# Performance work log

Measured on AMD Instinct MI355X. Metric: run time of the kernel, lower is better.

The kernel has to match this reference:

```python
import jax, jax.numpy as jnp
import numpy as np

LAMBDA = 25.0
MU = 25.0
NU = 1.0
ALPHA = 0.25
EPS = 1e-4
NUM_MATCHES = (20, 4)


def _cdist(x, y):
    # x: (B, L1, C), y: (B, L2, C) -> (B, L1, L2) euclidean distances
    x2 = jnp.sum(x * x, axis=-1)[..., :, None]
    y2 = jnp.sum(y * y, axis=-1)[..., None, :]
    d2 = x2 + y2 - 2.0 * jnp.einsum('blc,bmc->blm', x, y)
    return jnp.sqrt(jnp.maximum(d2, 0.0))


def _nearest_neighbors(input_maps, candidate_maps, distances, num_matches):
    # For each input location, its nearest candidate; then keep the
    # num_matches input locations with smallest NN distance, in original order.
    nn_dist = jnp.min(distances, axis=-1)    # (B, L1)
    nn_idx = jnp.argmin(distances, axis=-1)  # (B, L1)
    _, sel = jax.lax.top_k(-nn_dist, num_matches)  # (B, M) smallest distances
    sel = jnp.sort(sel, axis=1)  # restore original ordering of positions
    filtered_input = jnp.take_along_axis(input_maps, sel[..., None], axis=1)
    nn_sel = jnp.take_along_axis(nn_idx, sel, axis=1)
    filtered_candidate = jnp.take_along_axis(candidate_maps, nn_sel[..., None], axis=1)
    return filtered_input, filtered_candidate


def _mse(a, b):
    return jnp.mean((a - b) ** 2)


def _vicreg_loss(z_a, z_b):
    inv_loss = _mse(z_a, z_b)

    def var_loss(z):
        std = jnp.sqrt(jnp.var(z, axis=0, ddof=1) + EPS)
        return jnp.mean(jax.nn.relu(1.0 - std))

    def cov_loss(z):
        n, d = z.shape
        zc = z - jnp.mean(z, axis=0)
        cov = (zc.T @ zc) / (n - 1)
        off = cov - jnp.diag(jnp.diag(cov))
        return jnp.sum(off ** 2) / d

    v = 0.5 * (var_loss(z_a) + var_loss(z_b))
    c = cov_loss(z_a) + cov_loss(z_b)
    return LAMBDA * inv_loss + MU * v + NU * c


def _local_loss(z_global, z_local, grid_global, grid_local):
    B = z_global.shape[0]
    zg = z_global.reshape(B, -1, z_global.shape[-1])   # (B, Lg, C)
    zl = z_local.reshape(B, -1, z_local.shape[-1])     # (B, Ll, C)

    inv_loss = 0.0
    # feature-space NN
    gf, gn = _nearest_neighbors(zg, zl, _cdist(zg, zl), NUM_MATCHES[0])
    lf, ln = _nearest_neighbors(zl, zg, _cdist(zl, zg), NUM_MATCHES[1])
    inv_loss = inv_loss + (_mse(gf, gn) / 2 + _mse(lf, ln) / 2)

    # grid-space NN (distances from grids, gather from feature maps)
    gg = grid_global.reshape(B, -1, 2)
    gl = grid_local.reshape(B, -1, 2)
    gf, gn = _nearest_neighbors(zg, zl, _cdist(gg, gl), NUM_MATCHES[0])
    lf, ln = _nearest_neighbors(zl, zg, _cdist(gl, gg), NUM_MATCHES[1])
    inv_loss = inv_loss + (_mse(gf, gn) / 2 + _mse(lf, ln) / 2)

    return LAMBDA * inv_loss


def setup_inputs() -> dict:
    key = jax.random.key(0)
    ks = jax.random.split(key, 6)
    B, D, C = 32, 8192, 512
    return {
        'z_global': jax.random.normal(ks[0], (B, D), jnp.float32),
        'z_local': jax.random.normal(ks[1], (B, D), jnp.float32),
        'z_global_local_features': jax.random.normal(ks[2], (B, 24, 24, C), jnp.float32),
        'z_local_local_features': jax.random.normal(ks[3], (B, 16, 16, C), jnp.float32),
        'grid_global': jax.random.uniform(ks[4], (B, 24, 24, 2), jnp.float32),
        'grid_local': jax.random.uniform(ks[5], (B, 16, 16, 2), jnp.float32),
    }


def reference(z_global, z_local, z_global_local_features, z_local_local_features, grid_global, grid_local):
    global_loss = _vicreg_loss(z_global, z_local)
    local_loss = _local_loss(z_global_local_features, z_local_local_features, grid_global, grid_local)
    return ALPHA * global_loss + (1.0 - ALPHA) * local_loss
```

## Files before the change

### kernel.cpp

```cpp
#include <hip/hip_runtime.h>
#include <hip/hip_bf16.h>

#define BATCH 32
#define DZ    8192
#define LG    576
#define LL    256
#define CH    512

#define OFF_S      0
#define OFF_BSUM   8192
#define OFF_SELSUM 9472
#define OFF_DONE   10496
#define OFF_RNP    10560
#define OFF_CNP    305472
#define WS_NEED    895296

typedef __attribute__((ext_vector_type(8))) short bf16x8;
typedef __attribute__((ext_vector_type(4))) float f32x4;

__device__ __forceinline__ unsigned short f2bf(float x) {
  union { __hip_bfloat16 h; unsigned short u; } cv;
  cv.h = __float2bfloat16(x);
  return cv.u;
}

__device__ __forceinline__ uint4 pack8(float4 lo, float4 hi) {
  union { unsigned short h[8]; uint4 u; } pk;
  pk.h[0] = f2bf(lo.x); pk.h[1] = f2bf(lo.y); pk.h[2] = f2bf(lo.z); pk.h[3] = f2bf(lo.w);
  pk.h[4] = f2bf(hi.x); pk.h[5] = f2bf(hi.y); pk.h[6] = f2bf(hi.z); pk.h[7] = f2bf(hi.w);
  return pk.u;
}

__device__ __forceinline__ float dot4(float4 v) {
  return v.x * v.x + v.y * v.y + v.z * v.z + v.w * v.w;
}

struct SelSmem {
  unsigned long long keys[LG];
  unsigned int nnm[LG];
  float cxy[2 * LG];
  unsigned int plist[40];
  unsigned int cnt;
  float fred[4];
};

template <int V>
__device__ __forceinline__ void sel_case(
    SelSmem& sm, int b,
    const float* __restrict__ zgf, const float* __restrict__ zlf,
    const float* __restrict__ gg, const float* __restrict__ gl,
    const unsigned long long* __restrict__ rowNNp,
    const unsigned long long* __restrict__ colNNp,
    double* __restrict__ selsum) {
  constexpr bool GDIR = (V == 0 || V == 2);
  constexpr int L1 = GDIR ? LG : LL;
  constexpr int L2 = GDIR ? LL : LG;
  constexpr int M  = GDIR ? 20 : 4;
  constexpr int NR = (L1 + 255) / 256;
  const float* fin  = GDIR ? zgf + (size_t)b * LG * CH : zlf + (size_t)b * LL * CH;
  const float* fcan = GDIR ? zlf + (size_t)b * LL * CH : zgf + (size_t)b * LG * CH;
  int tid = threadIdx.x, lane = tid & 63, wv = tid >> 6;
  if (tid == 0) sm.cnt = 0;

  if constexpr (V < 2) {
    constexpr int P = (V == 0) ? 2 : 9;
    const unsigned long long* src =
        (V == 0) ? rowNNp + (size_t)b * LG * 2 : colNNp + (size_t)b * LL * 9;
    #pragma unroll
    for (int s = 0; s < NR; ++s) {
      int l = tid + s * 256;
      if (l < L1) {
        const unsigned long long* q = src + (size_t)l * P;
        unsigned long long p = q[0];
        #pragma unroll
        for (int u = 1; u < P; ++u) { unsigned long long t2 = q[u]; p = t2 < p ? t2 : p; }
        sm.keys[l] = (p & 0xFFFFFFFF00000000ull) | (unsigned)l;
        sm.nnm[l] = (unsigned)(p & 0xFFFFFFFFu);
      }
    }
  } else {
    const float* gin  = (V == 2) ? gg + (size_t)b * LG * 2 : gl + (size_t)b * LL * 2;
    const float* gcan = (V == 2) ? gl + (size_t)b * LL * 2 : gg + (size_t)b * LG * 2;
    #pragma unroll
    for (int s = 0; s < (2 * L2 + 255) / 256; ++s) {
      int i = tid + s * 256;
      if (i < 2 * L2) sm.cxy[i] = gcan[i];
    }
    __syncthreads();
    float x[NR], y[NR], bd[NR];
    unsigned bi[NR];
    #pragma unroll
    for (int s = 0; s < NR; ++s) {
      int l = tid + s * 256;
      x[s] = (l < L1) ? gin[2 * l] : 0.f;
      y[s] = (l < L1) ? gin[2 * l + 1] : 0.f;
      bd[s] = 3.4e38f; bi[s] = 0;
    }
    const float2* c2 = (const float2*)sm.cxy;
    for (int m2 = 0; m2 < L2; m2 += 8) {
      float2 cc[8];
      #pragma unroll
      for (int u = 0; u < 8; ++u) cc[u] = c2[m2 + u];
      #pragma unroll
      for (int u = 0; u < 8; ++u)
        #pragma unroll
        for (int s = 0; s < NR; ++s) {
          float dx = x[s] - cc[u].x, dy = y[s] - cc[u].y;
          float d2 = dx * dx + dy * dy;
          if (d2 < bd[s]) { bd[s] = d2; bi[s] = (unsigned)(m2 + u); }
        }
    }
    #pragma unroll
    for (int s = 0; s < NR; ++s) {
      int l = tid + s * 256;
      if (l < L1) {
        sm.keys[l] = ((unsigned long long)__float_as_uint(bd[s]) << 32) | (unsigned)l;
        sm.nnm[l] = bi[s];
      }
    }
  }
  __syncthreads();

  unsigned long long myk[NR];
  int rk[NR];
  #pragma unroll
  for (int s = 0; s < NR; ++s) {
    int l = tid + s * 256;
    myk[s] = (l < L1) ? sm.keys[l] : ~0ull;
    rk[s] = 0;
  }
  for (int j = 0; j < L1; j += 8) {
    unsigned long long kk[8];
    #pragma unroll
    for (int u = 0; u < 8; ++u) kk[u] = sm.keys[j + u];
    #pragma unroll
    for (int u = 0; u < 8; ++u)
      #pragma unroll
      for (int s = 0; s < NR; ++s) rk[s] += (kk[u] < myk[s]) ? 1 : 0;
  }
  #pragma unroll
  for (int s = 0; s < NR; ++s) {
    int l = tid + s * 256;
    if (l < L1 && rk[s] < M) {
      unsigned slot = atomicAdd(&sm.cnt, 1u);
      sm.plist[2 * slot] = (unsigned)l;
      sm.plist[2 * slot + 1] = sm.nnm[l];
    }
  }
  __syncthreads();

  float part = 0.f;
  #pragma unroll
  for (int rr = 0; rr < M / 4; ++rr) {
    int r = wv + rr * 4;
    const float4* a4 = (const float4*)(fin + (size_t)sm.plist[2 * r] * CH);
    const float4* c4 = (const float4*)(fcan + (size_t)sm.plist[2 * r + 1] * CH);
    float4 xa = a4[lane * 2], xb = a4[lane * 2 + 1];
    float4 ya = c4[lane * 2], yb = c4[lane * 2 + 1];
    float d0 = xa.x - ya.x, d1 = xa.y - ya.y, d2 = xa.z - ya.z, d3 = xa.w - ya.w;
    float d4 = xb.x - yb.x, d5 = xb.y - yb.y, d6 = xb.z - yb.z, d7 = xb.w - yb.w;
    part += d0 * d0 + d1 * d1 + d2 * d2 + d3 * d3 +
            d4 * d4 + d5 * d5 + d6 * d6 + d7 * d7;
  }
  for (int s = 32; s; s >>= 1) part += __shfl_down(part, s);
  if (lane == 0) sm.fred[wv] = part;
  __syncthreads();
  if (tid == 0)
    selsum[V * 32 + b] = (double)(sm.fred[0] + sm.fred[1] + sm.fred[2] + sm.fred[3]);
}

__global__ __launch_bounds__(256) void k_mega(
    const float* __restrict__ za, const float* __restrict__ zb,
    const float* __restrict__ zgf, const float* __restrict__ zlf,
    const float* __restrict__ gg, const float* __restrict__ gl,
    double* __restrict__ bsum, float* __restrict__ S,
    unsigned long long* __restrict__ rowNNp, unsigned long long* __restrict__ colNNp,
    double* __restrict__ selsum, unsigned int* __restrict__ doneCnt) {
  __shared__ __align__(16) char smem[28416];
  int tid = threadIdx.x, lane = tid & 63, wv = tid >> 6;
  int blk = blockIdx.x;

  if (blk < 576) {
    int fs = (blk & 7) * 72 + (blk >> 3);
    int b = fs / 18, rr_ = fs % 18;
    int by = rr_ / 9, bx = rr_ % 9;
    int row0 = bx * 64, col0 = by * 128;

    unsigned short (*As)[72] = (unsigned short(*)[72])smem;
    unsigned short (*Bs)[72] = (unsigned short(*)[72])(smem + 9216);
    float* Asn = (float*)(smem + 27648);
    float* Bsn = (float*)(smem + 27904);

    const int m16 = lane & 15, quad = lane >> 4;
    const int wm = wv >> 1, wn = wv & 1;
    const float* Ag = zgf + ((size_t)(b * LG + row0)) * CH;
    const float* Bg = zlf + ((size_t)(b * LL + col0)) * CH;
    const int sr = tid >> 2, sq = tid & 3;
    const int br = tid >> 1, bq = tid & 1;

    f32x4 acc[2][4] = {};
    float ssA = 0.f, ssB = 0.f;

    for (int k0 = 0; k0 < CH; k0 += 64) {
      const float* ap = Ag + (size_t)sr * CH + k0 + sq * 16;
      float4 a0 = *(const float4*)(ap);
      float4 a1 = *(const float4*)(ap + 4);
      float4 a2 = *(const float4*)(ap + 8);
      float4 a3 = *(const float4*)(ap + 12);
      const float* bp = Bg + (size_t)br * CH + k0 + bq * 16;
      float4 b0 = *(const float4*)(bp);
      float4 b1 = *(const float4*)(bp + 4);
      float4 b2 = *(const float4*)(bp + 8);
      float4 b3 = *(const float4*)(bp + 12);
      float4 b4 = *(const float4*)(bp + 32);
      float4 b5 = *(const float4*)(bp + 36);
      float4 b6 = *(const float4*)(bp + 40);
      float4 b7 = *(const float4*)(bp + 44);
      ssA += dot4(a0) + dot4(a1) + dot4(a2) + dot4(a3);
      ssB += dot4(b0) + dot4(b1) + dot4(b2) + dot4(b3) +
             dot4(b4) + dot4(b5) + dot4(b6) + dot4(b7);
      __syncthreads();
      *(uint4*)&As[sr][sq * 16]      = pack8(a0, a1);
      *(uint4*)&As[sr][sq * 16 + 8]  = pack8(a2, a3);
      *(uint4*)&Bs[br][bq * 16]      = pack8(b0, b1);
      *(uint4*)&Bs[br][bq * 16 + 8]  = pack8(b2, b3);
      *(uint4*)&Bs[br][bq * 16 + 32] = pack8(b4, b5);
      *(uint4*)&Bs[br][bq * 16 + 40] = pack8(b6, b7);
      __syncthreads();
      #pragma unroll
      for (int kk = 0; kk < 64; kk += 32) {
        bf16x8 af0 = *(const bf16x8*)&As[wm * 32 + m16][kk + quad * 8];
        bf16x8 af1 = *(const bf16x8*)&As[wm * 32 + 16 + m16][kk + quad * 8];
        bf16x8 bfv[4];
        #pragma unroll
        for (int j = 0; j < 4; ++j)
          bfv[j] = *(const bf16x8*)&Bs[wn * 64 + j * 16 + m16][kk + quad * 8];
        #pragma unroll
        for (int j = 0; j < 4; ++j) {
          acc[0][j] = __builtin_amdgcn_mfma_f32_16x16x32_bf16(af0, bfv[j], acc[0][j], 0, 0, 0);
          acc[1][j] = __builtin_amdgcn_mfma_f32_16x16x32_bf16(af1, bfv[j], acc[1][j], 0, 0, 0);
        }
      }
    }

    ssA += __shfl_xor(ssA, 1); ssA += __shfl_xor(ssA, 2);
    ssB += __shfl_xor(ssB, 1);
    if (sq == 0) Asn[sr] = ssA;
    if (bq == 0) Bsn[br] = ssB;
    __syncthreads();

    float na[2][4], nb[4];
    #pragma unroll
    for (int i = 0; i < 2; ++i)
      #pragma unroll
      for (int r = 0; r < 4; ++r)
        na[i][r] = Asn[wm * 32 + i * 16 + quad * 4 + r];
    #pragma unroll
    for (int j = 0; j < 4; ++j)
      nb[j] = Bsn[wn * 64 + j * 16 + m16];

    #pragma unroll
    for (int i = 0; i < 2; ++i) {
      #pragma unroll
      for (int r = 0; r < 4; ++r) {
        unsigned long long p = ~0ull;
        #pragma unroll
        for (int j = 0; j < 4; ++j) {
          float d = fmaxf(na[i][r] + nb[j] - 2.f * acc[i][j][r], 0.f);
          unsigned c = (unsigned)(col0 + wn * 64 + j * 16 + m16);
          unsigned long long pj = (((unsigned long long)__float_as_uint(d)) << 32) | c;
          p = pj < p ? pj : p;
        }
        #pragma unroll
        for (int s = 1; s < 16; s <<= 1) {
          unsigned long long q = __shfl_xor(p, s);
          p = q < p ? q : p;
        }
        if (m16 == 0)
          rowNNp[((size_t)b * LG + row0 + wm * 32 + i * 16 + quad * 4 + r) * 2 + by] = p;
      }
    }
    #pragma unroll
    for (int j = 0; j < 4; ++j) {
      unsigned long long p = ~0ull;
      #pragma unroll
      for (int i = 0; i < 2; ++i) {
        #pragma unroll
        for (int r = 0; r < 4; ++r) {
          float d = fmaxf(na[i][r] + nb[j] - 2.f * acc[i][j][r], 0.f);
          unsigned rg = (unsigned)(row0 + wm * 32 + i * 16 + quad * 4 + r);
          unsigned long long pr = (((unsigned long long)__float_as_uint(d)) << 32) | rg;
          p = pr < p ? pr : p;
        }
      }
      unsigned long long q = __shfl_xor(p, 16); p = q < p ? q : p;
      q = __shfl_xor(p, 32); p = q < p ? q : p;
      if (quad == 0)
        colNNp[((size_t)b * LL + col0 + wn * 64 + j * 16 + m16) * 9 + bx] = p;
    }
    return;
  }

  if (blk < 608) {
    float (*sred)[5] = (float(*)[5])smem;
    int blkS = blk - 576;
    if (blkS == 0 && tid == 0) *doneCnt = 0;
    int i = blkS * 256 + tid;
    float sa = 0.f, qa = 0.f, sb = 0.f, qb = 0.f, si = 0.f;
    #pragma unroll 8
    for (int b = 0; b < BATCH; ++b) {
      float va = za[(size_t)b * DZ + i];
      float vb = zb[(size_t)b * DZ + i];
      sa += va; qa += va * va;
      sb += vb; qb += vb * vb;
      float d = va - vb; si += d * d;
    }
    float ssa = qa - sa * sa * (1.f / 32.f);
    float ssb = qb - sb * sb * (1.f / 32.f);
    float v0 = si;
    float v1 = fmaxf(0.f, 1.f - sqrtf(ssa * (1.f / 31.f) + 1e-4f));
    float v2 = fmaxf(0.f, 1.f - sqrtf(ssb * (1.f / 31.f) + 1e-4f));
    float v3 = ssa * ssa, v4 = ssb * ssb;
    for (int off = 32; off; off >>= 1) {
      v0 += __shfl_down(v0, off); v1 += __shfl_down(v1, off);
      v2 += __shfl_down(v2, off); v3 += __shfl_down(v3, off);
      v4 += __shfl_down(v4, off);
    }
    if (lane == 0) {
      sred[wv][0] = v0; sred[wv][1] = v1; sred[wv][2] = v2;
      sred[wv][3] = v3; sred[wv][4] = v4;
    }
    __syncthreads();
    if (tid < 5)
      bsum[blkS * 5 + tid] =
          (double)(sred[0][tid] + sred[1][tid] + sred[2][tid] + sred[3][tid]);
    return;
  }

  if (blk < 1664) {
    float (*sred)[5] = (float(*)[5])smem;
    int e = blk - 608;
    int zi = e >= 528; if (zi) e -= 528;
    const float* z = zi ? zb : za;
    float* Sz = S + zi * 1024;
    int p = 0, rem = e;
    while (rem >= 32 - p) { rem -= 32 - p; ++p; }
    int q = p + rem;
    const float4* zp = (const float4*)(z + (size_t)p * DZ);
    const float4* zq = (const float4*)(z + (size_t)q * DZ);
    float s = 0.f;
    #pragma unroll
    for (int ii = 0; ii < 8; ++ii) {
      int i = tid + ii * 256;
      float4 a = zp[i], bb = zq[i];
      s += a.x * bb.x + a.y * bb.y + a.z * bb.z + a.w * bb.w;
    }
    for (int off = 32; off; off >>= 1) s += __shfl_down(s, off);
    if (lane == 0) sred[wv][0] = s;
    __syncthreads();
    if (tid == 0) {
      float r = sred[0][0] + sred[1][0] + sred[2][0] + sred[3][0];
      Sz[p * 32 + q] = r;
      if (p != q) Sz[q * 32 + p] = r;
    }
    return;
  }

  {
    SelSmem& sm = *reinterpret_cast<SelSmem*>(smem);
    int e = blk - 1664;
    int b2 = e >> 1;
    if (e & 1) sel_case<3>(sm, b2, zgf, zlf, gg, gl, rowNNp, colNNp, selsum);
    else       sel_case<2>(sm, b2, zgf, zlf, gg, gl, rowNNp, colNNp, selsum);
  }
}

struct TailSmem {
  SelSmem sel;
  float t[2][32];
  double sacc[5];
  double smf[4];
  int isLast;
};

__global__ __launch_bounds__(256) void k_tail(
    const float* __restrict__ zgf, const float* __restrict__ zlf,
    const float* __restrict__ gg, const float* __restrict__ gl,
    const unsigned long long* __restrict__ rowNNp,
    const unsigned long long* __restrict__ colNNp,
    double* __restrict__ selsum, const double* __restrict__ bsum,
    const float* __restrict__ S, unsigned int* __restrict__ doneCnt,
    float* __restrict__ out) {
  __shared__ TailSmem ts;
  int tid = threadIdx.x;
  int b = blockIdx.x >> 1, V = blockIdx.x & 1;
  if (V == 0) sel_case<0>(ts.sel, b, zgf, zlf, gg, gl, rowNNp, colNNp, selsum);
  else        sel_case<1>(ts.sel, b, zgf, zlf, gg, gl, rowNNp, colNNp, selsum);

  if (tid == 0) {
    __threadfence();
    unsigned r = atomicAdd(doneCnt, 1u);
    ts.isLast = (r == 63) ? 1 : 0;
  }
  __syncthreads();
  if (!ts.isLast) return;
  __threadfence();

  if (tid < 32) {
    #pragma unroll
    for (int zi = 0; zi < 2; ++zi) {
      float tp = 0.f;
      for (int bb = 0; bb < 32; ++bb) tp += S[zi * 1024 + tid * 32 + bb];
      ts.t[zi][tid] = tp * (1.f / 32.f);
    }
  }
  if (tid < 5) {
    double s = 0.0;
    for (int blk = 0; blk < 32; ++blk) s += bsum[blk * 5 + tid];
    ts.sacc[tid] = s;
  }
  if (tid >= 8 && tid < 12) {
    int v = tid - 8;
    double s = 0.0;
    for (int bb = 0; bb < 32; ++bb) s += selsum[v * 32 + bb];
    ts.smf[v] = s;
  }
  __syncthreads();
  if (tid < 64) {
    double total[2];
    #pragma unroll
    for (int zi = 0; zi < 2; ++zi) {
      float u = 0.f;
      for (int bb = 0; bb < 32; ++bb) u += ts.t[zi][bb];
      u *= (1.f / 32.f);
      double s = 0.0;
      for (int e = tid; e < 1024; e += 64) {
        int p = e >> 5, q = e & 31;
        float G = S[zi * 1024 + e] - ts.t[zi][p] - ts.t[zi][q] + u;
        s += (double)G * (double)G;
      }
      for (int off = 32; off; off >>= 1) s += __shfl_down(s, off);
      total[zi] = s;
    }
    if (tid == 0) {
      double inv_g = ts.sacc[0] / (32.0 * 8192.0);
      double v = 0.5 * (ts.sacc[1] + ts.sacc[2]) / 8192.0;
      double c = (total[0] - ts.sacc[3] + total[1] - ts.sacc[4]) / (961.0 * 8192.0);
      double gloss = 25.0 * inv_g + 25.0 * v + c;
      double mfg = ts.smf[0] / (32.0 * 20.0 * 512.0);
      double mfl = ts.smf[1] / (32.0 * 4.0 * 512.0);
      double mgg = ts.smf[2] / (32.0 * 20.0 * 512.0);
      double mgl = ts.smf[3] / (32.0 * 4.0 * 512.0);
      double lloss = 25.0 * (0.5 * (mfg + mfl) + 0.5 * (mgg + mgl));
      out[0] = (float)(0.25 * gloss + 0.75 * lloss);
    }
  }
}

extern "C" void kernel_launch(void* const* d_in, const int* in_sizes, int n_in,
                              void* d_out, int out_size, void* d_ws, size_t ws_size,
                              hipStream_t stream) {
  const float* zg  = (const float*)d_in[0];
  const float* zl  = (const float*)d_in[1];
  const float* zgf = (const float*)d_in[2];
  const float* zlf = (const float*)d_in[3];
  const float* gg  = (const float*)d_in[4];
  const float* glo = (const float*)d_in[5];

  char* ws = (char*)d_ws;
  float* S       = (float*)(ws + OFF_S);
  double* bsum   = (double*)(ws + OFF_BSUM);
  double* selsum = (double*)(ws + OFF_SELSUM);
  unsigned int* doneCnt = (unsigned int*)(ws + OFF_DONE);
  unsigned long long* rowNNp = (unsigned long long*)(ws + OFF_RNP);
  unsigned long long* colNNp = (unsigned long long*)(ws + OFF_CNP);

  k_mega<<<1728, 256, 0, stream>>>(zg, zl, zgf, zlf, gg, glo,
                                   bsum, S, rowNNp, colNNp, selsum, doneCnt);
  k_tail<<<64, 256, 0, stream>>>(zgf, zlf, gg, glo, rowNNp, colNNp,
                                 selsum, bsum, S, doneCnt, (float*)d_out);
}
```

Baseline: 159.4 us.

## Precast features to bf16 in a prepass and pipeline the GEMM with atomic NN merge

A new front kernel converts both feature maps to bf16 in workspace, computes row norms and initialises the nearest-neighbour slots. The distance GEMM then loads bf16 tiles and prefetches the next k-slice into registers while the current one is computed. Per-tile partial minima are merged with 64-bit atomicMin instead of being written to a partials array. The feature-space selection blocks now run inside the GEMM kernel and spin-wait on a completion counter. This removes per-tile conversion and norm work and the partial reduction, at the cost of writing and re-reading an extra bf16 copy of the features and relying on all spinning blocks being co-resident.

Result: slower. 225.6 us (+41.5%).

```diff
diff --git a/kernel.cpp b/kernel.cpp
--- a/kernel.cpp
+++ b/kernel.cpp
@@ -10,10 +10,14 @@
 #define OFF_S      0
 #define OFF_BSUM   8192
 #define OFF_SELSUM 9472
-#define OFF_DONE   10496
-#define OFF_RNP    10560
-#define OFF_CNP    305472
-#define WS_NEED    895296
+#define OFF_CNT    10496
+#define OFF_NG     10560
+#define OFF_NL     84288
+#define OFF_RNN    117056
+#define OFF_CNN    264512
+#define OFF_ABF    330048
+#define OFF_BBF    19204416
+#define WS_NEED    27593024
 
 typedef __attribute__((ext_vector_type(8))) short bf16x8;
 typedef __attribute__((ext_vector_type(4))) float f32x4;
@@ -22,17 +26,6 @@
   union { __hip_bfloat16 h; unsigned short u; } cv;
   cv.h = __float2bfloat16(x);
   return cv.u;
-}
-
-__device__ __forceinline__ uint4 pack8(float4 lo, float4 hi) {
-  union { unsigned short h[8]; uint4 u; } pk;
-  pk.h[0] = f2bf(lo.x); pk.h[1] = f2bf(lo.y); pk.h[2] = f2bf(lo.z); pk.h[3] = f2bf(lo.w);
-  pk.h[4] = f2bf(hi.x); pk.h[5] = f2bf(hi.y); pk.h[6] = f2bf(hi.z); pk.h[7] = f2bf(hi.w);
-  return pk.u;
-}
-
-__device__ __forceinline__ float dot4(float4 v) {
-  return v.x * v.x + v.y * v.y + v.z * v.z + v.w * v.w;
 }
 
 struct SelSmem {
@@ -49,8 +42,8 @@
     SelSmem& sm, int b,
     const float* __restrict__ zgf, const float* __restrict__ zlf,
     const float* __restrict__ gg, const float* __restrict__ gl,
-    const unsigned long long* __restrict__ rowNNp,
-    const unsigned long long* __restrict__ colNNp,
+    const unsigned long long* __restrict__ rowNN,
+    const unsigned long long* __restrict__ colNN,
     double* __restrict__ selsum) {
   constexpr bool GDIR = (V == 0 || V == 2);
   constexpr int L1 = GDIR ? LG : LL;
@@ -63,17 +56,13 @@
   if (tid == 0) sm.cnt = 0;
 
   if constexpr (V < 2) {
-    constexpr int P = (V == 0) ? 2 : 9;
     const unsigned long long* src =
-        (V == 0) ? rowNNp + (size_t)b * LG * 2 : colNNp + (size_t)b * LL * 9;
+        (V == 0) ? rowNN + (size_t)b * LG : colNN + (size_t)b * LL;
     #pragma unroll
     for (int s = 0; s < NR; ++s) {
       int l = tid + s * 256;
       if (l < L1) {
-        const unsigned long long* q = src + (size_t)l * P;
-        unsigned long long p = q[0];
-        #pragma unroll
-        for (int u = 1; u < P; ++u) { unsigned long long t2 = q[u]; p = t2 < p ? t2 : p; }
+        unsigned long long p = src[l];
         sm.keys[l] = (p & 0xFFFFFFFF00000000ull) | (unsigned)l;
         sm.nnm[l] = (unsigned)(p & 0xFFFFFFFFu);
       }
@@ -169,14 +158,141 @@
     selsum[V * 32 + b] = (double)(sm.fred[0] + sm.fred[1] + sm.fred[2] + sm.fred[3]);
 }
 
-__global__ __launch_bounds__(256) void k_mega(
+#define NPREP 6656
+__global__ __launch_bounds__(256) void k_front2(
     const float* __restrict__ za, const float* __restrict__ zb,
     const float* __restrict__ zgf, const float* __restrict__ zlf,
     const float* __restrict__ gg, const float* __restrict__ gl,
     double* __restrict__ bsum, float* __restrict__ S,
-    unsigned long long* __restrict__ rowNNp, unsigned long long* __restrict__ colNNp,
-    double* __restrict__ selsum, unsigned int* __restrict__ doneCnt) {
-  __shared__ __align__(16) char smem[28416];
+    unsigned short* __restrict__ Abf, unsigned short* __restrict__ Bbf,
+    float* __restrict__ ng, float* __restrict__ nl,
+    unsigned long long* __restrict__ nnInit,
+    unsigned int* __restrict__ cnt,
+    double* __restrict__ selsum) {
+  __shared__ __align__(16) char smem[12032];
+  int tid = threadIdx.x, lane = tid & 63, wv = tid >> 6;
+  int blk = blockIdx.x;
+
+  if (blk < NPREP) {
+    if (blk == 0 && tid == 0) {
+      __hip_atomic_store(&cnt[0], 0u, __ATOMIC_RELAXED, __HIP_MEMORY_SCOPE_AGENT);
+      __hip_atomic_store(&cnt[1], 0u, __ATOMIC_RELAXED, __HIP_MEMORY_SCOPE_AGENT);
+    }
+    int row = blk * 4 + wv;
+    if (lane == 0) nnInit[row] = ~0ull;
+    const float* src; unsigned short* dst; float* nrm;
+    if (row < BATCH * LG) {
+      src = zgf + (size_t)row * CH; dst = Abf + (size_t)row * CH; nrm = ng + row;
+    } else {
+      int rr = row - BATCH * LG;
+      src = zlf + (size_t)rr * CH; dst = Bbf + (size_t)rr * CH; nrm = nl + rr;
+    }
+    const float4* s4 = (const float4*)src;
+    float4 v0 = s4[lane * 2], v1 = s4[lane * 2 + 1];
+    float ss = v0.x * v0.x + v0.y * v0.y + v0.z * v0.z + v0.w * v0.w +
+               v1.x * v1.x + v1.y * v1.y + v1.z * v1.z + v1.w * v1.w;
+    union { unsigned short h[8]; uint4 u; } pk;
+    pk.h[0] = f2bf(v0.x); pk.h[1] = f2bf(v0.y); pk.h[2] = f2bf(v0.z); pk.h[3] = f2bf(v0.w);
+    pk.h[4] = f2bf(v1.x); pk.h[5] = f2bf(v1.y); pk.h[6] = f2bf(v1.z); pk.h[7] = f2bf(v1.w);
+    *(uint4*)(dst + lane * 8) = pk.u;
+    for (int off = 32; off; off >>= 1) ss += __shfl_down(ss, off);
+    if (lane == 0) *nrm = ss;
+    return;
+  }
+
+  if (blk < NPREP + 32) {
+    float (*sred)[5] = (float(*)[5])smem;
+    int blkS = blk - NPREP;
+    int i = blkS * 256 + tid;
+    float sa = 0.f, qa = 0.f, sb = 0.f, qb = 0.f, si = 0.f;
+    #pragma unroll 8
+    for (int b = 0; b < BATCH; ++b) {
+      float va = za[(size_t)b * DZ + i];
+      float vb = zb[(size_t)b * DZ + i];
+      sa += va; qa += va * va;
+      sb += vb; qb += vb * vb;
+      float d = va - vb; si += d * d;
+    }
+    float ssa = qa - sa * sa * (1.f / 32.f);
+    float ssb = qb - sb * sb * (1.f / 32.f);
+    float v0 = si;
+    float v1 = fmaxf(0.f, 1.f - sqrtf(ssa * (1.f / 31.f) + 1e-4f));
+    float v2 = fmaxf(0.f, 1.f - sqrtf(ssb * (1.f / 31.f) + 1e-4f));
+    float v3 = ssa * ssa, v4 = ssb * ssb;
+    for (int off = 32; off; off >>= 1) {
+      v0 += __shfl_down(v0, off); v1 += __shfl_down(v1, off);
+      v2 += __shfl_down(v2, off); v3 += __shfl_down(v3, off);
+      v4 += __shfl_down(v4, off);
+    }
+    if (lane == 0) {
+      sred[wv][0] = v0; sred[wv][1] = v1; sred[wv][2] = v2;
+      sred[wv][3] = v3; sred[wv][4] = v4;
+    }
+    __syncthreads();
+    if (tid < 5)
+      bsum[blkS * 5 + tid] =
+          (double)(sred[0][tid] + sred[1][tid] + sred[2][tid] + sred[3][tid]);
+    return;
+  }
+
+  if (blk < NPREP + 32 + 1056) {
+    float (*sred)[5] = (float(*)[5])smem;
+    int e = blk - (NPREP + 32);
+    int zi = e >= 528; if (zi) e -= 528;
+    const float* z = zi ? zb : za;
+    float* Sz = S + zi * 1024;
+    int p = 0, rem = e;
+    while (rem >= 32 - p) { rem -= 32 - p; ++p; }
+    int q = p + rem;
+    const float4* zp = (const float4*)(z + (size_t)p * DZ);
+    const float4* zq = (const float4*)(z + (size_t)q * DZ);
+    float s = 0.f;
+    #pragma unroll
+    for (int ii = 0; ii < 8; ++ii) {
+      int i = tid + ii * 256;
+      float4 a = zp[i], bb = zq[i];
+      s += a.x * bb.x + a.y * bb.y + a.z * bb.z + a.w * bb.w;
+    }
+    for (int off = 32; off; off >>= 1) s += __shfl_down(s, off);
+    if (lane == 0) sred[wv][0] = s;
+    __syncthreads();
+    if (tid == 0) {
+      float r = sred[0][0] + sred[1][0] + sred[2][0] + sred[3][0];
+      Sz[p * 32 + q] = r;
+      if (p != q) Sz[q * 32 + p] = r;
+    }
+    return;
+  }
+
+  {
+    SelSmem& sm = *reinterpret_cast<SelSmem*>(smem);
+    int e = blk - (NPREP + 32 + 1056);
+    int b2 = e >> 1;
+    if (e & 1) sel_case<3>(sm, b2, zgf, zlf, gg, gl, (const unsigned long long*)0,
+                           (const unsigned long long*)0, selsum);
+    else       sel_case<2>(sm, b2, zgf, zlf, gg, gl, (const unsigned long long*)0,
+                           (const unsigned long long*)0, selsum);
+  }
+}
+
+struct TailSmem {
+  SelSmem sel;
+  float t[2][32];
+  double sacc[5];
+  double smf[4];
+  int isLast;
+};
+
+__global__ __launch_bounds__(256) void k_back(
+    const float* __restrict__ zgf, const float* __restrict__ zlf,
+    const float* __restrict__ gg, const float* __restrict__ gl,
+    const unsigned short* __restrict__ Abf, const unsigned short* __restrict__ Bbf,
+    const float* __restrict__ ng, const float* __restrict__ nl,
+    unsigned long long* __restrict__ rowNN, unsigned long long* __restrict__ colNN,
+    double* __restrict__ selsum, const double* __restrict__ bsum,
+    const float* __restrict__ S, unsigned int* __restrict__ cnt,
+    float* __restrict__ out) {
+  __shared__ __align__(16) char smem[27904];
   int tid = threadIdx.x, lane = tid & 63, wv = tid >> 6;
   int blk = blockIdx.x;
 
@@ -188,45 +304,40 @@
 
     unsigned short (*As)[72] = (unsigned short(*)[72])smem;
     unsigned short (*Bs)[72] = (unsigned short(*)[72])(smem + 9216);
-    float* Asn = (float*)(smem + 27648);
-    float* Bsn = (float*)(smem + 27904);
 
     const int m16 = lane & 15, quad = lane >> 4;
     const int wm = wv >> 1, wn = wv & 1;
-    const float* Ag = zgf + ((size_t)(b * LG + row0)) * CH;
-    const float* Bg = zlf + ((size_t)(b * LL + col0)) * CH;
+    const unsigned short* Ag = Abf + ((size_t)(b * LG + row0)) * CH;
+    const unsigned short* Bg = Bbf + ((size_t)(b * LL + col0)) * CH;
     const int sr = tid >> 2, sq = tid & 3;
     const int br = tid >> 1, bq = tid & 1;
 
     f32x4 acc[2][4] = {};
-    float ssA = 0.f, ssB = 0.f;
-
-    for (int k0 = 0; k0 < CH; k0 += 64) {
-      const float* ap = Ag + (size_t)sr * CH + k0 + sq * 16;
-      float4 a0 = *(const float4*)(ap);
-      float4 a1 = *(const float4*)(ap + 4);
-      float4 a2 = *(const float4*)(ap + 8);
-      float4 a3 = *(const float4*)(ap + 12);
-      const float* bp = Bg + (size_t)br * CH + k0 + bq * 16;
-      float4 b0 = *(const float4*)(bp);
-      float4 b1 = *(const float4*)(bp + 4);
-      float4 b2 = *(const float4*)(bp + 8);
-      float4 b3 = *(const float4*)(bp + 12);
-      float4 b4 = *(const float4*)(bp + 32);
-      float4 b5 = *(const float4*)(bp + 36);
-      float4 b6 = *(const float4*)(bp + 40);
-      float4 b7 = *(const float4*)(bp + 44);
-      ssA += dot4(a0) + dot4(a1) + dot4(a2) + dot4(a3);
-      ssB += dot4(b0) + dot4(b1) + dot4(b2) + dot4(b3) +
-             dot4(b4) + dot4(b5) + dot4(b6) + dot4(b7);
+    uint4 a0, a1, b0, b1, b2, b3;
+
+    {
+      const unsigned short* ap = Ag + (size_t)sr * CH + sq * 16;
+      a0 = *(const uint4*)ap; a1 = *(const uint4*)(ap + 8);
+      const unsigned short* bp = Bg + (size_t)br * CH + bq * 16;
+      b0 = *(const uint4*)bp; b1 = *(const uint4*)(bp + 8);
+      b2 = *(const uint4*)(bp + 32); b3 = *(const uint4*)(bp + 40);
+    }
+
+    #pragma unroll
+    for (int t = 0; t < 8; ++t) {
       __syncthreads();
-      *(uint4*)&As[sr][sq * 16]      = pack8(a0, a1);
-      *(uint4*)&As[sr][sq * 16 + 8]  = pack8(a2, a3);
-      *(uint4*)&Bs[br][bq * 16]      = pack8(b0, b1);
-      *(uint4*)&Bs[br][bq * 16 + 8]  = pack8(b2, b3);
-      *(uint4*)&Bs[br][bq * 16 + 32] = pack8(b4, b5);
-      *(uint4*)&Bs[br][bq * 16 + 40] = pack8(b6, b7);
+      *(uint4*)&As[sr][sq * 16]      = a0; *(uint4*)&As[sr][sq * 16 + 8]  = a1;
+      *(uint4*)&Bs[br][bq * 16]      = b0; *(uint4*)&Bs[br][bq * 16 + 8]  = b1;
+      *(uint4*)&Bs[br][bq * 16 + 32] = b2; *(uint4*)&Bs[br][bq * 16 + 40] = b3;
       __syncthreads();
+      if (t < 7) {
+        int k0 = (t + 1) * 64;
+        const unsigned short* ap = Ag + (size_t)sr * CH + k0 + sq * 16;
+        a0 = *(const uint4*)ap; a1 = *(const uint4*)(ap + 8);
+        const unsigned short* bp = Bg + (size_t)br * CH + k0 + bq * 16;
+        b0 = *(const uint4*)bp; b1 = *(const uint4*)(bp + 8);
+        b2 = *(const uint4*)(bp + 32); b3 = *(const uint4*)(bp + 40);
+      }
       #pragma unroll
       for (int kk = 0; kk < 64; kk += 32) {
         bf16x8 af0 = *(const bf16x8*)&As[wm * 32 + m16][kk + quad * 8];
@@ -243,21 +354,15 @@
       }
     }
 
-    ssA += __shfl_xor(ssA, 1); ssA += __shfl_xor(ssA, 2);
-    ssB += __shfl_xor(ssB, 1);
-    if (sq == 0) Asn[sr] = ssA;
-    if (bq == 0) Bsn[br] = ssB;
-    __syncthreads();
-
     float na[2][4], nb[4];
     #pragma unroll
     for (int i = 0; i < 2; ++i)
       #pragma unroll
       for (int r = 0; r < 4; ++r)
-        na[i][r] = Asn[wm * 32 + i * 16 + quad * 4 + r];
+        na[i][r] = ng[b * LG + row0 + wm * 32 + i * 16 + quad * 4 + r];
     #pragma unroll
     for (int j = 0; j < 4; ++j)
-      nb[j] = Bsn[wn * 64 + j * 16 + m16];
+      nb[j] = nl[b * LL + col0 + wn * 64 + j * 16 + m16];
 
     #pragma unroll
     for (int i = 0; i < 2; ++i) {
@@ -277,7 +382,7 @@
           p = q < p ? q : p;
         }
         if (m16 == 0)
-          rowNNp[((size_t)b * LG + row0 + wm * 32 + i * 16 + quad * 4 + r) * 2 + by] = p;
+          atomicMin(&rowNN[(size_t)b * LG + row0 + wm * 32 + i * 16 + quad * 4 + r], p);
       }
     }
     #pragma unroll
@@ -296,110 +401,31 @@
       unsigned long long q = __shfl_xor(p, 16); p = q < p ? q : p;
       q = __shfl_xor(p, 32); p = q < p ? q : p;
       if (quad == 0)
-        colNNp[((size_t)b * LL + col0 + wn * 64 + j * 16 + m16) * 9 + bx] = p;
-    }
+        atomicMin(&colNN[(size_t)b * LL + col0 + wn * 64 + j * 16 + m16], p);
+    }
+
+    __syncthreads();
+    __threadfence();
+    if (tid == 0)
+      __hip_atomic_fetch_add(&cnt[0], 1u, __ATOMIC_RELEASE, __HIP_MEMORY_SCOPE_AGENT);
     return;
   }
 
-  if (blk < 608) {
-    float (*sred)[5] = (float(*)[5])smem;
-    int blkS = blk - 576;
-    if (blkS == 0 && tid == 0) *doneCnt = 0;
-    int i = blkS * 256 + tid;
-    float sa = 0.f, qa = 0.f, sb = 0.f, qb = 0.f, si = 0.f;
-    #pragma unroll 8
-    for (int b = 0; b < BATCH; ++b) {
-      float va = za[(size_t)b * DZ + i];
-      float vb = zb[(size_t)b * DZ + i];
-      sa += va; qa += va * va;
-      sb += vb; qb += vb * vb;
-      float d = va - vb; si += d * d;
-    }
-    float ssa = qa - sa * sa * (1.f / 32.f);
-    float ssb = qb - sb * sb * (1.f / 32.f);
-    float v0 = si;
-    float v1 = fmaxf(0.f, 1.f - sqrtf(ssa * (1.f / 31.f) + 1e-4f));
-    float v2 = fmaxf(0.f, 1.f - sqrtf(ssb * (1.f / 31.f) + 1e-4f));
-    float v3 = ssa * ssa, v4 = ssb * ssb;
-    for (int off = 32; off; off >>= 1) {
-      v0 += __shfl_down(v0, off); v1 += __shfl_down(v1, off);
-      v2 += __shfl_down(v2, off); v3 += __shfl_down(v3, off);
-      v4 += __shfl_down(v4, off);
-    }
-    if (lane == 0) {
-      sred[wv][0] = v0; sred[wv][1] = v1; sred[wv][2] = v2;
-      sred[wv][3] = v3; sred[wv][4] = v4;
-    }
-    __syncthreads();
-    if (tid < 5)
-      bsum[blkS * 5 + tid] =
-          (double)(sred[0][tid] + sred[1][tid] + sred[2][tid] + sred[3][tid]);
-    return;
-  }
-
-  if (blk < 1664) {
-    float (*sred)[5] = (float(*)[5])smem;
-    int e = blk - 608;
-    int zi = e >= 528; if (zi) e -= 528;
-    const float* z = zi ? zb : za;
-    float* Sz = S + zi * 1024;
-    int p = 0, rem = e;
-    while (rem >= 32 - p) { rem -= 32 - p; ++p; }
-    int q = p + rem;
-    const float4* zp = (const float4*)(z + (size_t)p * DZ);
-    const float4* zq = (const float4*)(z + (size_t)q * DZ);
-    float s = 0.f;
-    #pragma unroll
-    for (int ii = 0; ii < 8; ++ii) {
-      int i = tid + ii * 256;
-      float4 a = zp[i], bb = zq[i];
-      s += a.x * bb.x + a.y * bb.y + a.z * bb.z + a.w * bb.w;
-    }
-    for (int off = 32; off; off >>= 1) s += __shfl_down(s, off);
-    if (lane == 0) sred[wv][0] = s;
-    __syncthreads();
-    if (tid == 0) {
-      float r = sred[0][0] + sred[1][0] + sred[2][0] + sred[3][0];
-      Sz[p * 32 + q] = r;
-      if (p != q) Sz[q * 32 + p] = r;
-    }
-    return;
-  }
-
-  {
-    SelSmem& sm = *reinterpret_cast<SelSmem*>(smem);
-    int e = blk - 1664;
-    int b2 = e >> 1;
-    if (e & 1) sel_case<3>(sm, b2, zgf, zlf, gg, gl, rowNNp, colNNp, selsum);
-    else       sel_case<2>(sm, b2, zgf, zlf, gg, gl, rowNNp, colNNp, selsum);
-  }
-}
-
-struct TailSmem {
-  SelSmem sel;
-  float t[2][32];
-  double sacc[5];
-  double smf[4];
-  int isLast;
-};
-
-__global__ __launch_bounds__(256) void k_tail(
-    const float* __restrict__ zgf, const float* __restrict__ zlf,
-    const float* __restrict__ gg, const float* __restrict__ gl,
-    const unsigned long long* __restrict__ rowNNp,
-    const unsigned long long* __restrict__ colNNp,
-    double* __restrict__ selsum, const double* __restrict__ bsum,
-    const float* __restrict__ S, unsigned int* __restrict__ doneCnt,
-    float* __restrict__ out) {
-  __shared__ TailSmem ts;
-  int tid = threadIdx.x;
-  int b = blockIdx.x >> 1, V = blockIdx.x & 1;
-  if (V == 0) sel_case<0>(ts.sel, b, zgf, zlf, gg, gl, rowNNp, colNNp, selsum);
-  else        sel_case<1>(ts.sel, b, zgf, zlf, gg, gl, rowNNp, colNNp, selsum);
+  TailSmem& ts = *reinterpret_cast<TailSmem*>(smem);
+  if (tid == 0) {
+    while (__hip_atomic_load(&cnt[0], __ATOMIC_ACQUIRE, __HIP_MEMORY_SCOPE_AGENT) < 576u)
+      __builtin_amdgcn_s_sleep(8);
+  }
+  __syncthreads();
+
+  int e = blk - 576;
+  int b2 = e >> 1;
+  if (e & 1) sel_case<1>(ts.sel, b2, zgf, zlf, gg, gl, rowNN, colNN, selsum);
+  else       sel_case<0>(ts.sel, b2, zgf, zlf, gg, gl, rowNN, colNN, selsum);
 
   if (tid == 0) {
     __threadfence();
-    unsigned r = atomicAdd(doneCnt, 1u);
+    unsigned r = __hip_atomic_fetch_add(&cnt[1], 1u, __ATOMIC_ACQ_REL, __HIP_MEMORY_SCOPE_AGENT);
     ts.isLast = (r == 63) ? 1 : 0;
   }
   __syncthreads();
@@ -416,7 +442,7 @@
   }
   if (tid < 5) {
     double s = 0.0;
-    for (int blk = 0; blk < 32; ++blk) s += bsum[blk * 5 + tid];
+    for (int blk2 = 0; blk2 < 32; ++blk2) s += bsum[blk2 * 5 + tid];
     ts.sacc[tid] = s;
   }
   if (tid >= 8 && tid < 12) {
@@ -434,9 +460,9 @@
       for (int bb = 0; bb < 32; ++bb) u += ts.t[zi][bb];
       u *= (1.f / 32.f);
       double s = 0.0;
-      for (int e = tid; e < 1024; e += 64) {
-        int p = e >> 5, q = e & 31;
-        float G = S[zi * 1024 + e] - ts.t[zi][p] - ts.t[zi][q] + u;
+      for (int e2 = tid; e2 < 1024; e2 += 64) {
+        int p = e2 >> 5, q = e2 & 31;
+        float G = S[zi * 1024 + e2] - ts.t[zi][p] - ts.t[zi][q] + u;
         s += (double)G * (double)G;
       }
       for (int off = 32; off; off >>= 1) s += __shfl_down(s, off);
@@ -471,12 +497,16 @@
   float* S       = (float*)(ws + OFF_S);
   double* bsum   = (double*)(ws + OFF_BSUM);
   double* selsum = (double*)(ws + OFF_SELSUM);
-  unsigned int* doneCnt = (unsigned int*)(ws + OFF_DONE);
-  unsigned long long* rowNNp = (unsigned long long*)(ws + OFF_RNP);
-  unsigned long long* colNNp = (unsigned long long*)(ws + OFF_CNP);
-
-  k_mega<<<1728, 256, 0, stream>>>(zg, zl, zgf, zlf, gg, glo,
-                                   bsum, S, rowNNp, colNNp, selsum, doneCnt);
-  k_tail<<<64, 256, 0, stream>>>(zgf, zlf, gg, glo, rowNNp, colNNp,
-                                 selsum, bsum, S, doneCnt, (float*)d_out);
+  unsigned int* cnt = (unsigned int*)(ws + OFF_CNT);
+  float* ng = (float*)(ws + OFF_NG);
+  float* nl = (float*)(ws + OFF_NL);
+  unsigned long long* rowNN = (unsigned long long*)(ws + OFF_RNN);
+  unsigned long long* colNN = (unsigned long long*)(ws + OFF_CNN);
+  unsigned short* Abf = (unsigned short*)(ws + OFF_ABF);
+  unsigned short* Bbf = (unsigned short*)(ws + OFF_BBF);
+
+  k_front2<<<NPREP + 32 + 1056 + 64, 256, 0, stream>>>(
+      zg, zl, zgf, zlf, gg, glo, bsum, S, Abf, Bbf, ng, nl, rowNN, cnt, selsum);
+  k_back<<<640, 256, 0, stream>>>(zgf, zlf, gg, glo, Abf, Bbf, ng, nl,
+                                  rowNN, colNN, selsum, bsum, S, cnt, (float*)d_out);
 }
```

## Reorder mega-kernel block roles and prefetch next K-slice in distance GEMM

Applied to the files above, without the earlier changes.

The grid-space selection blocks (sel_case) now take the lowest block indices, so the long-running selection work is dispatched first instead of last. The Gram-matrix blocks move ahead of the variance/invariance blocks. In the feature-distance MFMA loop, the global loads for the next 64-wide K slice are issued after the LDS store, so they overlap with the MFMA work on the current slice. This raises register pressure and may lower occupancy.

Result: faster. 138.5 us (-13.1%).

```diff
diff --git a/kernel.cpp b/kernel.cpp
--- a/kernel.cpp
+++ b/kernel.cpp
@@ -10,7 +10,7 @@
 #define OFF_S      0
 #define OFF_BSUM   8192
 #define OFF_SELSUM 9472
-#define OFF_DONE   10496
+#define OFF_CNT    10496
 #define OFF_RNP    10560
 #define OFF_CNP    305472
 #define WS_NEED    895296
@@ -169,19 +169,28 @@
     selsum[V * 32 + b] = (double)(sm.fred[0] + sm.fred[1] + sm.fred[2] + sm.fred[3]);
 }
 
-__global__ __launch_bounds__(256) void k_mega(
+__global__ __launch_bounds__(256) void k_megaA(
     const float* __restrict__ za, const float* __restrict__ zb,
     const float* __restrict__ zgf, const float* __restrict__ zlf,
     const float* __restrict__ gg, const float* __restrict__ gl,
     double* __restrict__ bsum, float* __restrict__ S,
     unsigned long long* __restrict__ rowNNp, unsigned long long* __restrict__ colNNp,
-    double* __restrict__ selsum, unsigned int* __restrict__ doneCnt) {
+    double* __restrict__ selsum, unsigned int* __restrict__ cnt) {
   __shared__ __align__(16) char smem[28416];
   int tid = threadIdx.x, lane = tid & 63, wv = tid >> 6;
   int blk = blockIdx.x;
 
-  if (blk < 576) {
-    int fs = (blk & 7) * 72 + (blk >> 3);
+  if (blk < 64) {
+    SelSmem& sm = *reinterpret_cast<SelSmem*>(smem);
+    int b2 = blk >> 1;
+    if (blk & 1) sel_case<3>(sm, b2, zgf, zlf, gg, gl, rowNNp, colNNp, selsum);
+    else         sel_case<2>(sm, b2, zgf, zlf, gg, gl, rowNNp, colNNp, selsum);
+    return;
+  }
+
+  if (blk < 640) {
+    int fblk = blk - 64;
+    int fs = (fblk & 7) * 72 + (fblk >> 3);
     int b = fs / 18, rr_ = fs % 18;
     int by = rr_ / 9, bx = rr_ % 9;
     int row0 = bx * 64, col0 = by * 128;
@@ -200,25 +209,21 @@
 
     f32x4 acc[2][4] = {};
     float ssA = 0.f, ssB = 0.f;
-
-    for (int k0 = 0; k0 < CH; k0 += 64) {
-      const float* ap = Ag + (size_t)sr * CH + k0 + sq * 16;
-      float4 a0 = *(const float4*)(ap);
-      float4 a1 = *(const float4*)(ap + 4);
-      float4 a2 = *(const float4*)(ap + 8);
-      float4 a3 = *(const float4*)(ap + 12);
-      const float* bp = Bg + (size_t)br * CH + k0 + bq * 16;
-      float4 b0 = *(const float4*)(bp);
-      float4 b1 = *(const float4*)(bp + 4);
-      float4 b2 = *(const float4*)(bp + 8);
-      float4 b3 = *(const float4*)(bp + 12);
-      float4 b4 = *(const float4*)(bp + 32);
-      float4 b5 = *(const float4*)(bp + 36);
-      float4 b6 = *(const float4*)(bp + 40);
-      float4 b7 = *(const float4*)(bp + 44);
-      ssA += dot4(a0) + dot4(a1) + dot4(a2) + dot4(a3);
-      ssB += dot4(b0) + dot4(b1) + dot4(b2) + dot4(b3) +
-             dot4(b4) + dot4(b5) + dot4(b6) + dot4(b7);
+    float4 a0, a1, a2, a3, b0, b1, b2, b3, b4, b5, b6, b7;
+
+    {
+      const float* ap = Ag + (size_t)sr * CH + sq * 16;
+      a0 = *(const float4*)(ap);      a1 = *(const float4*)(ap + 4);
+      a2 = *(const float4*)(ap + 8);  a3 = *(const float4*)(ap + 12);
+      const float* bp = Bg + (size_t)br * CH + bq * 16;
+      b0 = *(const float4*)(bp);      b1 = *(const float4*)(bp + 4);
+      b2 = *(const float4*)(bp + 8);  b3 = *(const float4*)(bp + 12);
+      b4 = *(const float4*)(bp + 32); b5 = *(const float4*)(bp + 36);
+      b6 = *(const float4*)(bp + 40); b7 = *(const float4*)(bp + 44);
+    }
+
+    #pragma unroll
+    for (int t = 0; t < 8; ++t) {
       __syncthreads();
       *(uint4*)&As[sr][sq * 16]      = pack8(a0, a1);
       *(uint4*)&As[sr][sq * 16 + 8]  = pack8(a2, a3);
@@ -226,7 +231,21 @@
       *(uint4*)&Bs[br][bq * 16 + 8]  = pack8(b2, b3);
       *(uint4*)&Bs[br][bq * 16 + 32] = pack8(b4, b5);
       *(uint4*)&Bs[br][bq * 16 + 40] = pack8(b6, b7);
+      ssA += dot4(a0) + dot4(a1) + dot4(a2) + dot4(a3);
+      ssB += dot4(b0) + dot4(b1) + dot4(b2) + dot4(b3) +
+             dot4(b4) + dot4(b5) + dot4(b6) + dot4(b7);
       __syncthreads();
+      if (t < 7) {
+        int k0 = (t + 1) * 64;
+        const float* ap = Ag + (size_t)sr * CH + k0 + sq * 16;
+        a0 = *(const float4*)(ap);      a1 = *(const float4*)(ap + 4);
+        a2 = *(const float4*)(ap + 8);  a3 = *(const float4*)(ap + 12);
+        const float* bp = Bg + (size_t)br * CH + k0 + bq * 16;
+        b0 = *(const float4*)(bp);      b1 = *(const float4*)(bp + 4);
+        b2 = *(const float4*)(bp + 8);  b3 = *(const float4*)(bp + 12);
+        b4 = *(const float4*)(bp + 32); b5 = *(const float4*)(bp + 36);
+        b6 = *(const float4*)(bp + 40); b7 = *(const float4*)(bp + 44);
+      }
       #pragma unroll
       for (int kk = 0; kk < 64; kk += 32) {
         bf16x8 af0 = *(const bf16x8*)&As[wm * 32 + m16][kk + quad * 8];
@@ -301,10 +320,39 @@
     return;
   }
 
-  if (blk < 608) {
+  if (blk < 1696) {
     float (*sred)[5] = (float(*)[5])smem;
-    int blkS = blk - 576;
-    if (blkS == 0 && tid == 0) *doneCnt = 0;
+    int e = blk - 640;
+    int zi = e >= 528; if (zi) e -= 528;
+    const float* z = zi ? zb : za;
+    float* Sz = S + zi * 1024;
+    int p = 0, rem = e;
+    while (rem >= 32 - p) { rem -= 32 - p; ++p; }
+    int q = p + rem;
+    const float4* zp = (const float4*)(z + (size_t)p * DZ);
+    const float4* zq = (const float4*)(z + (size_t)q * DZ);
+    float s = 0.f;
+    #pragma unroll
+    for (int ii = 0; ii < 8; ++ii) {
+      int i = tid + ii * 256;
+      float4 a = zp[i], bb = zq[i];
+      s += a.x * bb.x + a.y * bb.y + a.z * bb.z + a.w * bb.w;
+    }
+    for (int off = 32; off; off >>= 1) s += __shfl_down(s, off);
+    if (lane == 0) sred[wv][0] = s;
+    __syncthreads();
+    if (tid == 0) {
+      float r = sred[0][0] + sred[1][0] + sred[2][0] + sred[3][0];
+      Sz[p * 32 + q] = r;
+      if (p != q) Sz[q * 32 + p] = r;
+    }
+    return;
+  }
+
+  {
+    float (*sred)[5] = (float(*)[5])smem;
+    int blkS = blk - 1696;
+    if (blkS == 0 && tid == 0) cnt[0] = 0;
     int i = blkS * 256 + tid;
     float sa = 0.f, qa = 0.f, sb = 0.f, qb = 0.f, si = 0.f;
     #pragma unroll 8
@@ -334,44 +382,6 @@
     if (tid < 5)
       bsum[blkS * 5 + tid] =
           (double)(sred[0][tid] + sred[1][tid] + sred[2][tid] + sred[3][tid]);
-    return;
-  }
-
-  if (blk < 1664) {
-    float (*sred)[5] = (float(*)[5])smem;
-    int e = blk - 608;
-    int zi = e >= 528; if (zi) e -= 528;
-    const float* z = zi ? zb : za;
-    float* Sz = S + zi * 1024;
-    int p = 0, rem = e;
-    while (rem >= 32 - p) { rem -= 32 - p; ++p; }
-    int q = p + rem;
-    const float4* zp = (const float4*)(z + (size_t)p * DZ);
-    const float4* zq = (const float4*)(z + (size_t)q * DZ);
-    float s = 0.f;
-    #pragma unroll
-    for (int ii = 0; ii < 8; ++ii) {
-      int i = tid + ii * 256;
-      float4 a = zp[i], bb = zq[i];
-      s += a.x * bb.x + a.y * bb.y + a.z * bb.z + a.w * bb.w;
-    }
-    for (int off = 32; off; off >>= 1) s += __shfl_down(s, off);
-    if (lane == 0) sred[wv][0] = s;
-    __syncthreads();
-    if (tid == 0) {
-      float r = sred[0][0] + sred[1][0] + sred[2][0] + sred[3][0];
-      Sz[p * 32 + q] = r;
-      if (p != q) Sz[q * 32 + p] = r;
-    }
-    return;
-  }
-
-  {
-    SelSmem& sm = *reinterpret_cast<SelSmem*>(smem);
-    int e = blk - 1664;
-    int b2 = e >> 1;
-    if (e & 1) sel_case<3>(sm, b2, zgf, zlf, gg, gl, rowNNp, colNNp, selsum);
-    else       sel_case<2>(sm, b2, zgf, zlf, gg, gl, rowNNp, colNNp, selsum);
   }
 }
 
@@ -416,7 +426,7 @@
   }
   if (tid < 5) {
     double s = 0.0;
-    for (int blk = 0; blk < 32; ++blk) s += bsum[blk * 5 + tid];
+    for (int blk2 = 0; blk2 < 32; ++blk2) s += bsum[blk2 * 5 + tid];
     ts.sacc[tid] = s;
   }
   if (tid >= 8 && tid < 12) {
@@ -434,9 +444,9 @@
       for (int bb = 0; bb < 32; ++bb) u += ts.t[zi][bb];
       u *= (1.f / 32.f);
       double s = 0.0;
-      for (int e = tid; e < 1024; e += 64) {
-        int p = e >> 5, q = e & 31;
-        float G = S[zi * 1024 + e] - ts.t[zi][p] - ts.t[zi][q] + u;
+      for (int e2 = tid; e2 < 1024; e2 += 64) {
+        int p = e2 >> 5, q = e2 & 31;
+        float G = S[zi * 1024 + e2] - ts.t[zi][p] - ts.t[zi][q] + u;
         s += (double)G * (double)G;
       }
       for (int off = 32; off; off >>= 1) s += __shfl_down(s, off);
@@ -471,12 +481,12 @@
   float* S       = (float*)(ws + OFF_S);
   double* bsum   = (double*)(ws + OFF_BSUM);
   double* selsum = (double*)(ws + OFF_SELSUM);
-  unsigned int* doneCnt = (unsigned int*)(ws + OFF_DONE);
+  unsigned int* cnt = (unsigned int*)(ws + OFF_CNT);
   unsigned long long* rowNNp = (unsigned long long*)(ws + OFF_RNP);
   unsigned long long* colNNp = (unsigned long long*)(ws + OFF_CNP);
 
-  k_mega<<<1728, 256, 0, stream>>>(zg, zl, zgf, zlf, gg, glo,
-                                   bsum, S, rowNNp, colNNp, selsum, doneCnt);
+  k_megaA<<<1728, 256, 0, stream>>>(zg, zl, zgf, zlf, gg, glo,
+                                    bsum, S, rowNNp, colNNp, selsum, cnt);
   k_tail<<<64, 256, 0, stream>>>(zgf, zlf, gg, glo, rowNNp, colNNp,
-                                 selsum, bsum, S, doneCnt, (float*)d_out);
-}
+                                 selsum, bsum, S, cnt, (float*)d_out);
+}
```
